# Performance work log

Hardware: AMD Instinct MI355X
Metric: run time of the kernel (lower is better)

The kernel has to match this reference:

```python
import jax, jax.numpy as jnp
import numpy as np

B, P, C = 64, 8732, 81
NEG_POS_RATIO = 3.0
NEG_LABEL_IDX = 0


def setup_inputs() -> dict:
    key = jax.random.key(0)
    k1, k2, k3, k4, k5 = jax.random.split(key, 5)
    confidence = jax.random.normal(k1, (B, P, C), dtype=jnp.float32)
    pred_loc = jax.random.normal(k2, (B, P, 4), dtype=jnp.float32)
    gt_bbox_loc = jax.random.normal(k3, (B, P, 4), dtype=jnp.float32)
    fg = jax.random.uniform(k4, (B, P)) < 0.03
    cls = jax.random.randint(k5, (B, P), 1, C)
    gt_class_labels = jnp.where(fg, cls, 0).astype(jnp.int32)
    return {"confidence": confidence, "pred_loc": pred_loc,
            "gt_class_labels": gt_class_labels, "gt_bbox_loc": gt_bbox_loc}


def hard_negative_mining(predicted_prob, gt_label, neg_pos_ratio):
    # predicted_prob, gt_label: (B, P)
    pos_flag = gt_label > 0
    prob = jnp.where(pos_flag, -1.0, predicted_prob)  # exclude positives from mining
    indices = jnp.argsort(-prob, axis=1)              # descending sort indices
    orders = jnp.argsort(indices, axis=1)             # rank of each prior in that sort
    num_pos = pos_flag.sum(axis=1, keepdims=True)
    num_neg = neg_pos_ratio * num_pos.astype(jnp.float32)
    neg_flag = orders.astype(jnp.float32) < num_neg
    return pos_flag, neg_flag


def reference(confidence, pred_loc, gt_class_labels, gt_bbox_loc):
    logp = jax.nn.log_softmax(confidence, axis=2)           # (B, P, C)
    # --- hard negative mining (no grad in original) ---
    neg_class_prob = -jax.lax.stop_gradient(logp)[:, :, NEG_LABEL_IDX]
    pos_flag, neg_flag = hard_negative_mining(neg_class_prob, gt_class_labels, NEG_POS_RATIO)
    sel_flag = pos_flag | neg_flag                          # (B, P)
    num_pos = pos_flag.sum(axis=1, keepdims=True).astype(jnp.float32)  # (B, 1)
    # --- masked cross entropy (mean over selected priors across whole batch) ---
    nll = -jnp.take_along_axis(logp, gt_class_labels[..., None].astype(jnp.int32), axis=2)[..., 0]
    n_sel = jnp.maximum(sel_flag.sum().astype(jnp.float32), 1.0)
    ce = jnp.sum(jnp.where(sel_flag, nll, 0.0)) / n_sel
    conf_loss = ce / num_pos                                # (B, 1), as in original
    # --- smooth L1 localization loss over positive priors ---
    d = pred_loc - gt_bbox_loc
    ad = jnp.abs(d)
    sl1 = jnp.where(ad < 1.0, 0.5 * d * d, ad - 0.5)        # (B, P, 4)
    pos_f = pos_flag[..., None].astype(sl1.dtype)
    n_matched = jnp.maximum(pos_flag.sum().astype(jnp.float32), 1.0)
    loc_huber_loss = jnp.sum(sl1 * pos_f) / n_matched
    return conf_loss, loc_huber_loss
```

## Files before the change

kernel.cpp:

```cpp
#include <hip/hip_runtime.h>
#include <cstdint>

#define BB 64
#define PP 8732
#define CC 81
#define PRB 128
#define TPB 512
#define NBX ((PP + PRB - 1) / PRB)

#define GLOBAL_AS __attribute__((address_space(1)))
#define LDS_AS __attribute__((address_space(3)))

__device__ __forceinline__ float wsum(float v) {
#pragma unroll
  for (int o = 32; o > 0; o >>= 1) v += __shfl_xor(v, o, 64);
  return v;
}
__device__ __forceinline__ int wsumi(int v) {
#pragma unroll
  for (int o = 32; o > 0; o >>= 1) v += __shfl_xor(v, o, 64);
  return v;
}

__global__ __launch_bounds__(TPB) void k_rowstats(
    const float* __restrict__ conf, const float* __restrict__ ploc,
    const int* __restrict__ label, const float* __restrict__ gloc,
    float* __restrict__ negp, int* __restrict__ part_cnt,
    float* __restrict__ part_nll, float* __restrict__ part_loc) {
  __shared__ float s_lin[PRB * CC];
  __shared__ float sh_n[TPB / 64], sh_l[TPB / 64];
  __shared__ int sh_c[TPB / 64];

  const int b = blockIdx.y;
  const int bx = blockIdx.x;
  const int p0 = bx * PRB;
  const int np = min(PRB, PP - p0);
  const int tid = threadIdx.x;
  const size_t rowbase = (size_t)b * PP + p0;
  const size_t gbase = rowbase * CC;

  {
    const GLOBAL_AS float* g = (const GLOBAL_AS float*)(conf + gbase);
    LDS_AS float* l = (LDS_AS float*)s_lin;
    const int n4 = (np * CC) >> 2;
    for (int i = tid; i < n4; i += TPB)
      __builtin_amdgcn_global_load_lds((const GLOBAL_AS void*)(g + 4 * i),
                                       (LDS_AS void*)(l + 4 * i), 16, 0, 0);
  }

  const int p = tid >> 2, q = tid & 3;
  const bool act = (p < np);
  int lab = 0;
  float df = 0.0f;
  if (act) {
    lab = label[rowbase + p];
    const size_t idx = rowbase * 4 + tid;
    df = ploc[idx] - gloc[idx];
  }
  __syncthreads();

  float nll_acc = 0.0f, loc_acc = 0.0f;
  int cnt = 0;
  if (act) {
    const float* xr = s_lin + p * CC;
    float s = 0.0f;
    for (int c = q; c < CC; c += 4) s += __expf(xr[c]);
    s += __shfl_xor(s, 1, 64);
    s += __shfl_xor(s, 2, 64);
    const float lse = __logf(s);

    const bool pos = lab > 0;
    const float ad = fabsf(df);
    loc_acc = pos ? ((ad < 1.0f) ? 0.5f * df * df : ad - 0.5f) : 0.0f;
    if (q == 0) {
      negp[rowbase + p] = pos ? 0.0f : fmaxf(lse - xr[0], 0.0f);
      if (pos) { cnt = 1; nll_acc = lse - xr[lab]; }
    }
  }

  const float na = wsum(nll_acc);
  const float la = wsum(loc_acc);
  const int ca = wsumi(cnt);
  const int wave = tid >> 6, lane = tid & 63;
  if (lane == 0) { sh_n[wave] = na; sh_l[wave] = la; sh_c[wave] = ca; }
  __syncthreads();
  if (tid == 0) {
    float tn = 0.0f, tl = 0.0f; int tc = 0;
#pragma unroll
    for (int w = 0; w < TPB / 64; ++w) { tn += sh_n[w]; tl += sh_l[w]; tc += sh_c[w]; }
    const int slot = b * NBX + bx;
    part_cnt[slot] = tc;
    part_nll[slot] = tn;
    part_loc[slot] = tl;
  }
}

#define RREP 16
#define HSTR 257
#define TTK 1024
__global__ __launch_bounds__(TTK) void k_topk(
    const float* __restrict__ negp, const int* __restrict__ part_cnt,
    const float* __restrict__ part_nll, const float* __restrict__ part_loc,
    int* __restrict__ row_npos, float* __restrict__ row_nll,
    float* __restrict__ row_loc, float* __restrict__ row_topk) {
  __shared__ uint32_t s_v[PP];
  __shared__ int s_hist[RREP * HSTR];
  __shared__ int s_tot[256];
  __shared__ uint32_t s_pref;
  __shared__ int s_kk;
  __shared__ int s_npos;
  __shared__ float s_redn[TTK / 64], s_redl[TTK / 64], s_redf[TTK / 64];
  __shared__ int s_redc[TTK / 64];

  const int b = blockIdx.x;
  const int tid = threadIdx.x;
  const int lane = tid & 63, wave = tid >> 6;

  {
    const GLOBAL_AS float* g = (const GLOBAL_AS float*)(negp + (size_t)b * PP);
    LDS_AS uint32_t* l = (LDS_AS uint32_t*)s_v;
    for (int i = tid; i < PP / 4; i += TTK)
      __builtin_amdgcn_global_load_lds((const GLOBAL_AS void*)(g + 4 * i),
                                       (LDS_AS void*)(l + 4 * i), 16, 0, 0);
  }

  {
    int c = 0; float n = 0.0f, l = 0.0f;
    if (tid < NBX) {
      const int slot = b * NBX + tid;
      c = part_cnt[slot]; n = part_nll[slot]; l = part_loc[slot];
    }
    const int cc = wsumi(c);
    const float nn = wsum(n);
    const float ll = wsum(l);
    if (lane == 0) { s_redc[wave] = cc; s_redn[wave] = nn; s_redl[wave] = ll; }
  }
  for (int i = tid; i < RREP * HSTR; i += TTK) s_hist[i] = 0;
  __syncthreads();
  if (tid == 0) {
    int tc = 0; float tn = 0.0f, tl = 0.0f;
#pragma unroll
    for (int w = 0; w < TTK / 64; ++w) { tc += s_redc[w]; tn += s_redn[w]; tl += s_redl[w]; }
    row_npos[b] = tc; row_nll[b] = tn; row_loc[b] = tl;
    s_npos = tc;
  }
  __syncthreads();

  const int npos = s_npos;
  int K = 3 * npos;
  const int mx = PP - npos;
  if (K > mx) K = mx;
  if (K <= 0) {
    if (tid == 0) row_topk[b] = 0.0f;
    return;
  }

  if (tid == 0) { s_pref = 0u; s_kk = K; }
  __syncthreads();
  const int rep = tid & (RREP - 1);

  for (int pass = 0; pass < 4; ++pass) {
    const int sh = 24 - 8 * pass;
    const uint32_t himask = (pass == 0) ? 0u : (0xFFFFFFFFu << (sh + 8));
    const uint32_t pref = s_pref;
    for (int i = tid; i < PP; i += TTK) {
      const uint32_t u = s_v[i];
      if ((u & himask) == (pref & himask))
        atomicAdd(&s_hist[rep * HSTR + ((u >> sh) & 0xFF)], 1);
    }
    __syncthreads();
    if (tid < 256) {
      int tt = 0;
#pragma unroll
      for (int r = 0; r < RREP; ++r) tt += s_hist[r * HSTR + tid];
      s_tot[tid] = tt;
    }
    __syncthreads();
    for (int i = tid; i < RREP * HSTR; i += TTK) s_hist[i] = 0;
    if (tid < 64) {
      const int l = tid;
      const int e0 = s_tot[4 * l], e1 = s_tot[4 * l + 1];
      const int e2 = s_tot[4 * l + 2], e3 = s_tot[4 * l + 3];
      const int L = e0 + e1 + e2 + e3;
      int x = L;
#pragma unroll
      for (int o = 1; o < 64; o <<= 1) {
        const int v = __shfl_down(x, o, 64);
        if (l + o < 64) x += v;
      }
      const int T = x - L;
      const int S3 = e3 + T, S2 = e2 + S3, S1 = e1 + S2, S0 = e0 + S1;
      const int kk = s_kk;
      const uint32_t pf = s_pref;
      if (S0 >= kk && S1 < kk) { s_pref = pf | ((uint32_t)(4 * l + 0) << sh); s_kk = kk - S1; }
      if (S1 >= kk && S2 < kk) { s_pref = pf | ((uint32_t)(4 * l + 1) << sh); s_kk = kk - S2; }
      if (S2 >= kk && S3 < kk) { s_pref = pf | ((uint32_t)(4 * l + 2) << sh); s_kk = kk - S3; }
      if (S3 >= kk && T  < kk) { s_pref = pf | ((uint32_t)(4 * l + 3) << sh); s_kk = kk - T; }
    }
    __syncthreads();
  }

  const uint32_t T = s_pref;
  const int kk = s_kk;
  float local = 0.0f;
  for (int i = tid; i < PP; i += TTK) {
    const uint32_t u = s_v[i];
    if (u > T) local += __uint_as_float(u);
  }
  local = wsum(local);
  if (lane == 0) s_redf[wave] = local;
  __syncthreads();
  if (tid == 0) {
    float tot = 0.0f;
#pragma unroll
    for (int w = 0; w < TTK / 64; ++w) tot += s_redf[w];
    row_topk[b] = tot + (float)kk * __uint_as_float(T);
  }
}

__global__ void k_final(const int* __restrict__ row_npos, const float* __restrict__ row_nll,
                        const float* __restrict__ row_loc, const float* __restrict__ row_topk,
                        float* __restrict__ out) {
  const int lane = threadIdx.x;
  const int npos = row_npos[lane];
  const float nll = row_nll[lane] + row_topk[lane];
  const float loc = row_loc[lane];
  int K = 3 * npos;
  const int mx = PP - npos;
  if (K > mx) K = mx;
  const float nsel = (float)(npos + K);

  const float tot_nll = wsum(nll);
  const float tot_loc = wsum(loc);
  const float tot_pos = wsum((float)npos);
  const float tot_sel = wsum(nsel);

  const float ce = tot_nll / fmaxf(tot_sel, 1.0f);
  out[lane] = ce / (float)npos;
  if (lane == 0) out[BB] = tot_loc / fmaxf(tot_pos, 1.0f);
}

extern "C" void kernel_launch(void* const* d_in, const int* in_sizes, int n_in,
                              void* d_out, int out_size, void* d_ws, size_t ws_size,
                              hipStream_t stream) {
  const float* conf = (const float*)d_in[0];
  const float* ploc = (const float*)d_in[1];
  const int* label = (const int*)d_in[2];
  const float* gloc = (const float*)d_in[3];
  float* out = (float*)d_out;

  float* negp = (float*)d_ws;
  int* part_cnt = (int*)(negp + (size_t)BB * PP);
  float* part_nll = (float*)(part_cnt + BB * NBX);
  float* part_loc = part_nll + BB * NBX;
  int* row_npos = (int*)(part_loc + BB * NBX);
  float* row_nll = (float*)(row_npos + BB);
  float* row_loc = row_nll + BB;
  float* row_topk = row_loc + BB;

  dim3 g1(NBX, BB);
  hipLaunchKernelGGL(k_rowstats, g1, dim3(TPB), 0, stream,
                     conf, ploc, label, gloc, negp, part_cnt, part_nll, part_loc);
  hipLaunchKernelGGL(k_topk, dim3(BB), dim3(TTK), 0, stream,
                     negp, part_cnt, part_nll, part_loc,
                     row_npos, row_nll, row_loc, row_topk);
  hipLaunchKernelGGL(k_final, dim3(1), dim3(64), 0, stream,
                     row_npos, row_nll, row_loc, row_topk, out);
}
```

Measured before the change: 277.9 us.

## Fuse all three kernels into one cooperative persistent kernel with double-buffered tiles

Replaces the three launches with one cooperative kernel of 256 blocks (four per batch row), separated by grid syncs. Each block streams its quarter of the row through double-buffered LDS tiles, issuing the next tile's async global-to-LDS copy while the current one is processed. Then 64 blocks run the radix top-k and block 0 does the final reduction. This removes launch gaps and the partial-sum round trips, but the main streaming phase now runs on only 256 blocks of 1024 threads, which may not use all of the HBM bandwidth, and grid.sync itself has a cost.

```diff
diff --git a/kernel.cpp b/kernel.cpp
--- a/kernel.cpp
+++ b/kernel.cpp
@@ -1,16 +1,22 @@
 #include <hip/hip_runtime.h>
+#include <hip/hip_cooperative_groups.h>
 #include <cstdint>
 
 #define BB 64
 #define PP 8732
 #define CC 81
-#define PRB 128
-#define TPB 512
-#define NBX ((PP + PRB - 1) / PRB)
+#define QR 2183
+#define TILE 128
+#define NT 18
+#define TAIL 7
+#define NBLK 256
+#define NTHR 1024
 
 #define GLOBAL_AS __attribute__((address_space(1)))
 #define LDS_AS __attribute__((address_space(3)))
 
+namespace cg = cooperative_groups;
+
 __device__ __forceinline__ float wsum(float v) {
 #pragma unroll
   for (int o = 32; o > 0; o >>= 1) v += __shfl_xor(v, o, 64);
@@ -22,222 +28,218 @@
   return v;
 }
 
-__global__ __launch_bounds__(TPB) void k_rowstats(
+__device__ __forceinline__ void dma_floats(const float* gsrc, float* ldst,
+                                           int nf, int tid) {
+  const GLOBAL_AS float* g = (const GLOBAL_AS float*)gsrc;
+  LDS_AS float* l = (LDS_AS float*)ldst;
+  const int n4 = nf >> 2;
+  for (int i = tid; i < n4; i += NTHR)
+    __builtin_amdgcn_global_load_lds((const GLOBAL_AS void*)(g + 4 * i),
+                                     (LDS_AS void*)(l + 4 * i), 16, 0, 0);
+  const int rem = nf & 3;
+  if (tid < rem)
+    __builtin_amdgcn_global_load_lds((const GLOBAL_AS void*)(g + 4 * n4 + tid),
+                                     (LDS_AS void*)(l + 4 * n4 + tid), 4, 0, 0);
+}
+
+#define RREP 16
+#define HSTR 257
+
+__global__ __launch_bounds__(NTHR, 1) void k_fused(
     const float* __restrict__ conf, const float* __restrict__ ploc,
     const int* __restrict__ label, const float* __restrict__ gloc,
     float* __restrict__ negp, int* __restrict__ part_cnt,
-    float* __restrict__ part_nll, float* __restrict__ part_loc) {
-  __shared__ float s_lin[PRB * CC];
-  __shared__ float sh_n[TPB / 64], sh_l[TPB / 64];
-  __shared__ int sh_c[TPB / 64];
-
-  const int b = blockIdx.y;
-  const int bx = blockIdx.x;
-  const int p0 = bx * PRB;
-  const int np = min(PRB, PP - p0);
-  const int tid = threadIdx.x;
-  const size_t rowbase = (size_t)b * PP + p0;
-  const size_t gbase = rowbase * CC;
-
-  {
-    const GLOBAL_AS float* g = (const GLOBAL_AS float*)(conf + gbase);
-    LDS_AS float* l = (LDS_AS float*)s_lin;
-    const int n4 = (np * CC) >> 2;
-    for (int i = tid; i < n4; i += TPB)
-      __builtin_amdgcn_global_load_lds((const GLOBAL_AS void*)(g + 4 * i),
-                                       (LDS_AS void*)(l + 4 * i), 16, 0, 0);
-  }
-
-  const int p = tid >> 2, q = tid & 3;
-  const bool act = (p < np);
-  int lab = 0;
-  float df = 0.0f;
-  if (act) {
-    lab = label[rowbase + p];
-    const size_t idx = rowbase * 4 + tid;
-    df = ploc[idx] - gloc[idx];
-  }
-  __syncthreads();
-
-  float nll_acc = 0.0f, loc_acc = 0.0f;
-  int cnt = 0;
-  if (act) {
-    const float* xr = s_lin + p * CC;
-    float s = 0.0f;
-    for (int c = q; c < CC; c += 4) s += __expf(xr[c]);
-    s += __shfl_xor(s, 1, 64);
-    s += __shfl_xor(s, 2, 64);
-    const float lse = __logf(s);
-
-    const bool pos = lab > 0;
-    const float ad = fabsf(df);
-    loc_acc = pos ? ((ad < 1.0f) ? 0.5f * df * df : ad - 0.5f) : 0.0f;
-    if (q == 0) {
-      negp[rowbase + p] = pos ? 0.0f : fmaxf(lse - xr[0], 0.0f);
-      if (pos) { cnt = 1; nll_acc = lse - xr[lab]; }
-    }
-  }
-
-  const float na = wsum(nll_acc);
-  const float la = wsum(loc_acc);
-  const int ca = wsumi(cnt);
-  const int wave = tid >> 6, lane = tid & 63;
-  if (lane == 0) { sh_n[wave] = na; sh_l[wave] = la; sh_c[wave] = ca; }
-  __syncthreads();
-  if (tid == 0) {
-    float tn = 0.0f, tl = 0.0f; int tc = 0;
-#pragma unroll
-    for (int w = 0; w < TPB / 64; ++w) { tn += sh_n[w]; tl += sh_l[w]; tc += sh_c[w]; }
-    const int slot = b * NBX + bx;
-    part_cnt[slot] = tc;
-    part_nll[slot] = tn;
-    part_loc[slot] = tl;
-  }
-}
-
-#define RREP 16
-#define HSTR 257
-#define TTK 1024
-__global__ __launch_bounds__(TTK) void k_topk(
-    const float* __restrict__ negp, const int* __restrict__ part_cnt,
-    const float* __restrict__ part_nll, const float* __restrict__ part_loc,
+    float* __restrict__ part_nll, float* __restrict__ part_loc,
     int* __restrict__ row_npos, float* __restrict__ row_nll,
-    float* __restrict__ row_loc, float* __restrict__ row_topk) {
-  __shared__ uint32_t s_v[PP];
-  __shared__ int s_hist[RREP * HSTR];
-  __shared__ int s_tot[256];
+    float* __restrict__ row_loc, float* __restrict__ row_topk,
+    float* __restrict__ out) {
+  __shared__ __align__(16) unsigned char s_mem[2 * TILE * CC * 4];
+  __shared__ float sh_n[NTHR / 64], sh_l[NTHR / 64], sh_f[NTHR / 64];
+  __shared__ int sh_c[NTHR / 64];
   __shared__ uint32_t s_pref;
-  __shared__ int s_kk;
-  __shared__ int s_npos;
-  __shared__ float s_redn[TTK / 64], s_redl[TTK / 64], s_redf[TTK / 64];
-  __shared__ int s_redc[TTK / 64];
-
-  const int b = blockIdx.x;
+  __shared__ int s_kk, s_npos;
+
+  cg::grid_group grid = cg::this_grid();
+
+  const int g = blockIdx.x;
+  const int b = g >> 2, qy = g & 3;
   const int tid = threadIdx.x;
   const int lane = tid & 63, wave = tid >> 6;
 
+  float* buf0 = (float*)s_mem;
+  float* buf1 = buf0 + TILE * CC;
+  const size_t rowbase = (size_t)b * PP + (size_t)qy * QR;
+  const float* cbase = conf + rowbase * CC;
+
+  dma_floats(cbase, buf0, TILE * CC, tid);
+
+  float loc_acc = 0.0f, nll_acc = 0.0f;
+  int cnt = 0;
+  for (int i = tid; i < QR * 4; i += NTHR) {
+    const int p = i >> 2;
+    const int lab = label[rowbase + p];
+    if (lab > 0) {
+      const size_t idx = rowbase * 4 + i;
+      const float df = ploc[idx] - gloc[idx];
+      const float ad = fabsf(df);
+      loc_acc += (ad < 1.0f) ? 0.5f * df * df : ad - 0.5f;
+      if ((i & 3) == 0) cnt++;
+    }
+  }
+
+  const int p_l = tid >> 3, q = tid & 7;
+  for (int t = 0; t < NT; ++t) {
+    __syncthreads();
+    if (t + 1 < NT) {
+      const int nf = (t + 1 == NT - 1) ? TAIL * CC : TILE * CC;
+      dma_floats(cbase + (size_t)(t + 1) * TILE * CC,
+                 ((t + 1) & 1) ? buf1 : buf0, nf, tid);
+    }
+    const int np = (t == NT - 1) ? TAIL : TILE;
+    if (p_l < np) {
+      const float* xr = ((t & 1) ? buf1 : buf0) + p_l * CC;
+      float s = 0.0f;
+      for (int c = q; c < CC; c += 8) s += __expf(xr[c]);
+      s += __shfl_xor(s, 1, 64);
+      s += __shfl_xor(s, 2, 64);
+      s += __shfl_xor(s, 4, 64);
+      if (q == 0) {
+        const float lse = __logf(s);
+        const int gp = t * TILE + p_l;
+        const int lab = label[rowbase + gp];
+        const bool pos = lab > 0;
+        negp[rowbase + gp] = pos ? 0.0f : fmaxf(lse - xr[0], 0.0f);
+        if (pos) nll_acc += lse - xr[lab];
+      }
+    }
+  }
+
   {
-    const GLOBAL_AS float* g = (const GLOBAL_AS float*)(negp + (size_t)b * PP);
-    LDS_AS uint32_t* l = (LDS_AS uint32_t*)s_v;
-    for (int i = tid; i < PP / 4; i += TTK)
-      __builtin_amdgcn_global_load_lds((const GLOBAL_AS void*)(g + 4 * i),
-                                       (LDS_AS void*)(l + 4 * i), 16, 0, 0);
-  }
-
-  {
-    int c = 0; float n = 0.0f, l = 0.0f;
-    if (tid < NBX) {
-      const int slot = b * NBX + tid;
-      c = part_cnt[slot]; n = part_nll[slot]; l = part_loc[slot];
-    }
-    const int cc = wsumi(c);
-    const float nn = wsum(n);
-    const float ll = wsum(l);
-    if (lane == 0) { s_redc[wave] = cc; s_redn[wave] = nn; s_redl[wave] = ll; }
-  }
-  for (int i = tid; i < RREP * HSTR; i += TTK) s_hist[i] = 0;
-  __syncthreads();
-  if (tid == 0) {
-    int tc = 0; float tn = 0.0f, tl = 0.0f;
-#pragma unroll
-    for (int w = 0; w < TTK / 64; ++w) { tc += s_redc[w]; tn += s_redn[w]; tl += s_redl[w]; }
-    row_npos[b] = tc; row_nll[b] = tn; row_loc[b] = tl;
-    s_npos = tc;
-  }
-  __syncthreads();
-
-  const int npos = s_npos;
-  int K = 3 * npos;
-  const int mx = PP - npos;
-  if (K > mx) K = mx;
-  if (K <= 0) {
-    if (tid == 0) row_topk[b] = 0.0f;
-    return;
-  }
-
-  if (tid == 0) { s_pref = 0u; s_kk = K; }
-  __syncthreads();
-  const int rep = tid & (RREP - 1);
-
-  for (int pass = 0; pass < 4; ++pass) {
-    const int sh = 24 - 8 * pass;
-    const uint32_t himask = (pass == 0) ? 0u : (0xFFFFFFFFu << (sh + 8));
-    const uint32_t pref = s_pref;
-    for (int i = tid; i < PP; i += TTK) {
-      const uint32_t u = s_v[i];
-      if ((u & himask) == (pref & himask))
-        atomicAdd(&s_hist[rep * HSTR + ((u >> sh) & 0xFF)], 1);
-    }
+    const float na = wsum(nll_acc);
+    const float la = wsum(loc_acc);
+    const int ca = wsumi(cnt);
+    if (lane == 0) { sh_n[wave] = na; sh_l[wave] = la; sh_c[wave] = ca; }
     __syncthreads();
-    if (tid < 256) {
-      int tt = 0;
-#pragma unroll
-      for (int r = 0; r < RREP; ++r) tt += s_hist[r * HSTR + tid];
-      s_tot[tid] = tt;
-    }
+    if (tid == 0) {
+      float tn = 0.0f, tl = 0.0f; int tc = 0;
+#pragma unroll
+      for (int w = 0; w < NTHR / 64; ++w) { tn += sh_n[w]; tl += sh_l[w]; tc += sh_c[w]; }
+      part_cnt[g] = tc; part_nll[g] = tn; part_loc[g] = tl;
+    }
+  }
+
+  grid.sync();
+
+  if (g < BB) {
+    uint32_t* s_v = (uint32_t*)s_mem;
+    int* s_hist = (int*)(s_mem + 34928);
+    int* s_tot = (int*)(s_mem + 34928 + 16448);
+
+    dma_floats(negp + (size_t)g * PP, (float*)s_v, PP, tid);
+
+    if (tid == 0) {
+      const int i4 = g * 4;
+      const int tc = part_cnt[i4] + part_cnt[i4 + 1] + part_cnt[i4 + 2] + part_cnt[i4 + 3];
+      const float tn = part_nll[i4] + part_nll[i4 + 1] + part_nll[i4 + 2] + part_nll[i4 + 3];
+      const float tl = part_loc[i4] + part_loc[i4 + 1] + part_loc[i4 + 2] + part_loc[i4 + 3];
+      row_npos[g] = tc; row_nll[g] = tn; row_loc[g] = tl;
+      s_npos = tc; s_pref = 0u;
+    }
+    for (int i = tid; i < RREP * HSTR; i += NTHR) s_hist[i] = 0;
     __syncthreads();
-    for (int i = tid; i < RREP * HSTR; i += TTK) s_hist[i] = 0;
-    if (tid < 64) {
-      const int l = tid;
-      const int e0 = s_tot[4 * l], e1 = s_tot[4 * l + 1];
-      const int e2 = s_tot[4 * l + 2], e3 = s_tot[4 * l + 3];
-      const int L = e0 + e1 + e2 + e3;
-      int x = L;
-#pragma unroll
-      for (int o = 1; o < 64; o <<= 1) {
-        const int v = __shfl_down(x, o, 64);
-        if (l + o < 64) x += v;
-      }
-      const int T = x - L;
-      const int S3 = e3 + T, S2 = e2 + S3, S1 = e1 + S2, S0 = e0 + S1;
+
+    const int npos = s_npos;
+    int K = 3 * npos;
+    const int mx = PP - npos;
+    if (K > mx) K = mx;
+
+    if (K > 0) {
+      if (tid == 0) s_kk = K;
+      __syncthreads();
+      const int rep = tid & (RREP - 1);
+
+      for (int pass = 0; pass < 4; ++pass) {
+        const int sh = 24 - 8 * pass;
+        const uint32_t himask = (pass == 0) ? 0u : (0xFFFFFFFFu << (sh + 8));
+        const uint32_t pref = s_pref;
+        for (int i = tid; i < PP; i += NTHR) {
+          const uint32_t u = s_v[i];
+          if ((u & himask) == (pref & himask))
+            atomicAdd(&s_hist[rep * HSTR + ((u >> sh) & 0xFF)], 1);
+        }
+        __syncthreads();
+        if (tid < 256) {
+          int tt = 0;
+#pragma unroll
+          for (int r = 0; r < RREP; ++r) tt += s_hist[r * HSTR + tid];
+          s_tot[tid] = tt;
+        }
+        __syncthreads();
+        for (int i = tid; i < RREP * HSTR; i += NTHR) s_hist[i] = 0;
+        if (tid < 64) {
+          const int l = tid;
+          const int e0 = s_tot[4 * l], e1 = s_tot[4 * l + 1];
+          const int e2 = s_tot[4 * l + 2], e3 = s_tot[4 * l + 3];
+          const int L = e0 + e1 + e2 + e3;
+          int x = L;
+#pragma unroll
+          for (int o = 1; o < 64; o <<= 1) {
+            const int v = __shfl_down(x, o, 64);
+            if (l + o < 64) x += v;
+          }
+          const int T = x - L;
+          const int S3 = e3 + T, S2 = e2 + S3, S1 = e1 + S2, S0 = e0 + S1;
+          const int kk = s_kk;
+          const uint32_t pf = s_pref;
+          if (S0 >= kk && S1 < kk) { s_pref = pf | ((uint32_t)(4 * l + 0) << sh); s_kk = kk - S1; }
+          if (S1 >= kk && S2 < kk) { s_pref = pf | ((uint32_t)(4 * l + 1) << sh); s_kk = kk - S2; }
+          if (S2 >= kk && S3 < kk) { s_pref = pf | ((uint32_t)(4 * l + 2) << sh); s_kk = kk - S3; }
+          if (S3 >= kk && T  < kk) { s_pref = pf | ((uint32_t)(4 * l + 3) << sh); s_kk = kk - T; }
+        }
+        __syncthreads();
+      }
+
+      const uint32_t T = s_pref;
       const int kk = s_kk;
-      const uint32_t pf = s_pref;
-      if (S0 >= kk && S1 < kk) { s_pref = pf | ((uint32_t)(4 * l + 0) << sh); s_kk = kk - S1; }
-      if (S1 >= kk && S2 < kk) { s_pref = pf | ((uint32_t)(4 * l + 1) << sh); s_kk = kk - S2; }
-      if (S2 >= kk && S3 < kk) { s_pref = pf | ((uint32_t)(4 * l + 2) << sh); s_kk = kk - S3; }
-      if (S3 >= kk && T  < kk) { s_pref = pf | ((uint32_t)(4 * l + 3) << sh); s_kk = kk - T; }
-    }
-    __syncthreads();
-  }
-
-  const uint32_t T = s_pref;
-  const int kk = s_kk;
-  float local = 0.0f;
-  for (int i = tid; i < PP; i += TTK) {
-    const uint32_t u = s_v[i];
-    if (u > T) local += __uint_as_float(u);
-  }
-  local = wsum(local);
-  if (lane == 0) s_redf[wave] = local;
-  __syncthreads();
-  if (tid == 0) {
-    float tot = 0.0f;
-#pragma unroll
-    for (int w = 0; w < TTK / 64; ++w) tot += s_redf[w];
-    row_topk[b] = tot + (float)kk * __uint_as_float(T);
-  }
-}
-
-__global__ void k_final(const int* __restrict__ row_npos, const float* __restrict__ row_nll,
-                        const float* __restrict__ row_loc, const float* __restrict__ row_topk,
-                        float* __restrict__ out) {
-  const int lane = threadIdx.x;
-  const int npos = row_npos[lane];
-  const float nll = row_nll[lane] + row_topk[lane];
-  const float loc = row_loc[lane];
-  int K = 3 * npos;
-  const int mx = PP - npos;
-  if (K > mx) K = mx;
-  const float nsel = (float)(npos + K);
-
-  const float tot_nll = wsum(nll);
-  const float tot_loc = wsum(loc);
-  const float tot_pos = wsum((float)npos);
-  const float tot_sel = wsum(nsel);
-
-  const float ce = tot_nll / fmaxf(tot_sel, 1.0f);
-  out[lane] = ce / (float)npos;
-  if (lane == 0) out[BB] = tot_loc / fmaxf(tot_pos, 1.0f);
+      float local = 0.0f;
+      for (int i = tid; i < PP; i += NTHR) {
+        const uint32_t u = s_v[i];
+        if (u > T) local += __uint_as_float(u);
+      }
+      local = wsum(local);
+      if (lane == 0) sh_f[wave] = local;
+      __syncthreads();
+      if (tid == 0) {
+        float tot = 0.0f;
+#pragma unroll
+        for (int w = 0; w < NTHR / 64; ++w) tot += sh_f[w];
+        row_topk[g] = tot + (float)kk * __uint_as_float(T);
+      }
+    } else {
+      if (tid == 0) row_topk[g] = 0.0f;
+    }
+  }
+
+  grid.sync();
+
+  if (g == 0 && tid < 64) {
+    const int npos = row_npos[tid];
+    const float nll = row_nll[tid] + row_topk[tid];
+    const float loc = row_loc[tid];
+    int K = 3 * npos;
+    const int mx = PP - npos;
+    if (K > mx) K = mx;
+    const float nsel = (float)(npos + K);
+
+    const float tot_nll = wsum(nll);
+    const float tot_loc = wsum(loc);
+    const float tot_pos = wsum((float)npos);
+    const float tot_sel = wsum(nsel);
+
+    const float ce = tot_nll / fmaxf(tot_sel, 1.0f);
+    out[tid] = ce / (float)npos;
+    if (tid == 0) out[BB] = tot_loc / fmaxf(tot_pos, 1.0f);
+  }
 }
 
 extern "C" void kernel_launch(void* const* d_in, const int* in_sizes, int n_in,
@@ -251,19 +253,18 @@
 
   float* negp = (float*)d_ws;
   int* part_cnt = (int*)(negp + (size_t)BB * PP);
-  float* part_nll = (float*)(part_cnt + BB * NBX);
-  float* part_loc = part_nll + BB * NBX;
-  int* row_npos = (int*)(part_loc + BB * NBX);
+  float* part_nll = (float*)(part_cnt + NBLK);
+  float* part_loc = part_nll + NBLK;
+  int* row_npos = (int*)(part_loc + NBLK);
   float* row_nll = (float*)(row_npos + BB);
   float* row_loc = row_nll + BB;
   float* row_topk = row_loc + BB;
 
-  dim3 g1(NBX, BB);
-  hipLaunchKernelGGL(k_rowstats, g1, dim3(TPB), 0, stream,
-                     conf, ploc, label, gloc, negp, part_cnt, part_nll, part_loc);
-  hipLaunchKernelGGL(k_topk, dim3(BB), dim3(TTK), 0, stream,
-                     negp, part_cnt, part_nll, part_loc,
-                     row_npos, row_nll, row_loc, row_topk);
-  hipLaunchKernelGGL(k_final, dim3(1), dim3(64), 0, stream,
-                     row_npos, row_nll, row_loc, row_topk, out);
-}
+  void* args[] = {
+      (void*)&conf, (void*)&ploc, (void*)&label, (void*)&gloc,
+      (void*)&negp, (void*)&part_cnt, (void*)&part_nll, (void*)&part_loc,
+      (void*)&row_npos, (void*)&row_nll, (void*)&row_loc, (void*)&row_topk,
+      (void*)&out};
+  hipLaunchCooperativeKernel((void*)k_fused, dim3(NBLK), dim3(NTHR),
+                             args, 0, stream);
+}
```

Measured after the change: 352.0 us. +26.7%, slower.
